# Performance work log

Measured on AMD Instinct MI355X. Metric: run time of the kernel, lower is better.

The kernel has to match this reference:

```python
import jax, jax.numpy as jnp
import numpy as np

D = 768
ED = 192  # d // 4
E = 8     # n_experts
K = 2     # top_k
B, H, W = 32, 32, 32
LN_EPS = 1e-5


def setup_inputs() -> dict:
    key = jax.random.key(0)
    ks = jax.random.split(key, 5)
    s = 0.02
    x = jax.random.normal(ks[0], (B, D, H, W), dtype=jnp.float32)
    Wr = jax.random.normal(ks[1], (E, D), dtype=jnp.float32) * s   # router: logits = tokens @ Wr.T
    W1 = jax.random.normal(ks[2], (E, D, ED), dtype=jnp.float32) * s  # gate proj (silu branch)
    W3 = jax.random.normal(ks[3], (E, D, ED), dtype=jnp.float32) * s  # linear branch
    W2 = jax.random.normal(ks[4], (E, ED, D), dtype=jnp.float32) * s  # down proj
    gamma = jnp.ones((D,), dtype=jnp.float32)
    beta = jnp.zeros((D,), dtype=jnp.float32)
    return {"x": x, "Wr": Wr, "W1": W1, "W3": W3, "W2": W2, "gamma": gamma, "beta": beta}


def _layernorm(y, gamma, beta):
    mu = jnp.mean(y, axis=-1, keepdims=True)
    var = jnp.mean(jnp.square(y - mu), axis=-1, keepdims=True)
    return (y - mu) * jax.lax.rsqrt(var + LN_EPS) * gamma + beta


def _moe_forward(x, Wr, W1, W3, W2, gamma, beta):
    b, c, h, w = x.shape
    tokens = x.transpose(0, 2, 3, 1).reshape(-1, c)        # [T, d]
    logits = tokens @ Wr.T                                  # [T, E]
    topk_v, topk_i = jax.lax.top_k(logits, K)               # [T, K]
    topk_w = jax.nn.softmax(topk_v, axis=-1)                # [T, K]
    # dense combine weights: zero for non-selected experts (same math as masked scatter)
    gates = jnp.sum(jax.nn.one_hot(topk_i, E, dtype=tokens.dtype) * topk_w[..., None], axis=1)  # [T, E]
    # SwiGLU per expert (forward uses silu(e[0](t)) * e[2](t), then e[3])
    hdn = jax.nn.silu(jnp.einsum('td,edh->teh', tokens, W1)) * jnp.einsum('td,edh->teh', tokens, W3)  # [T,E,ed]
    y = jnp.einsum('te,teh,ehd->td', gates, hdn, W2)        # combine: [T, d]
    out = _layernorm(y, gamma, beta) + tokens
    return out.reshape(b, h, w, c).transpose(0, 3, 1, 2)


def reference(x, Wr, W1, W3, W2, gamma, beta):
    return _moe_forward(x, Wr, W1, W3, W2, gamma, beta)
```

## Files before the change

### kernel.cpp

```cpp
#include <hip/hip_runtime.h>
#include <cstdint>
#include <cstddef>

#define T_TOK 32768
#define DM 768
#define EDIM 192
#define NEXP 8

typedef unsigned short u16;
typedef short bf16x8 __attribute__((ext_vector_type(8)));
typedef float f32x4 __attribute__((ext_vector_type(4)));
typedef u16 u16x8 __attribute__((ext_vector_type(8)));

__device__ __forceinline__ u16 f2bf(float f) {
  unsigned u = __float_as_uint(f);
  return (u16)((u + 0x7FFFu + ((u >> 16) & 1u)) >> 16);
}
__device__ __forceinline__ float bf2f(u16 u) {
  return __uint_as_float(((unsigned)u) << 16);
}

__device__ __forceinline__ void gld16(const void* g, void* l) {
  __builtin_amdgcn_global_load_lds(
      (const __attribute__((address_space(1))) unsigned int*)g,
      (__attribute__((address_space(3))) unsigned int*)l,
      16, 0, 0);
}

__device__ __forceinline__ bf16x8 frag_ld(const u16* lds, int row, int kb) {
  int ph = row * 128 + (kb ^ ((row & 7) << 4));
  return *(const bf16x8*)((const char*)lds + ph);
}

__global__ __launch_bounds__(256) void k_prep(
    const float* __restrict__ W1, const float* __restrict__ W3,
    const float* __restrict__ W2, u16* __restrict__ W1T,
    u16* __restrict__ W3T, u16* __restrict__ W2T)
{
  __shared__ __align__(16) float td[64][68];
  const int z = blockIdx.z;
  const int mat = z >> 3, e = z & 7;
  const int R = (mat == 2) ? EDIM : DM;
  const int C = (mat == 2) ? DM : EDIM;
  const int r0 = blockIdx.x * 64, c0 = blockIdx.y * 64;
  if (r0 >= R || c0 >= C) return;
  const float* in = (mat == 0 ? W1 : mat == 1 ? W3 : W2) + (size_t)e * R * C;
  u16* out = (mat == 0 ? W1T : mat == 1 ? W3T : W2T) + (size_t)e * R * C;
  const int tid = threadIdx.x;
  {
    int rl = tid >> 2, cs = (tid & 3) * 16;
    const float* s = in + (size_t)(r0 + rl) * C + c0 + cs;
    #pragma unroll
    for (int i = 0; i < 16; i += 4) *(float4*)&td[rl][cs + i] = *(const float4*)(s + i);
  }
  __syncthreads();
  {
    int cl = tid >> 2, rs = (tid & 3) * 16;
    u16* d = out + (size_t)(c0 + cl) * R + r0 + rs;
    u16x8 o0, o1;
    #pragma unroll
    for (int i = 0; i < 8; ++i) {
      o0[i] = f2bf(td[rs + i][cl]);
      o1[i] = f2bf(td[rs + 8 + i][cl]);
    }
    *(u16x8*)d = o0;
    *(u16x8*)(d + 8) = o1;
  }
}

__global__ __launch_bounds__(256) void k_tokrouter(
    const float* __restrict__ x, const float* __restrict__ Wr,
    u16* __restrict__ tokbf, int* __restrict__ cnt,
    int* __restrict__ toklist, float* __restrict__ gatelist)
{
  __shared__ float WrL[8][772];
  __shared__ float xL[64][33];
  __shared__ float logitsL[32][8];
  __shared__ int cnt8[8];
  __shared__ int baseL[8];
  const int tid = threadIdx.x;
  const int t0 = blockIdx.x * 32;
  const int b = t0 >> 10;
  const int h = (t0 >> 5) & 31;
  const float* xb = x + (size_t)b * (DM * 1024) + h * 32;

  for (int i = tid; i < 1536; i += 256) {
    int r = i / 192;
    int c = (i - r * 192) * 4;
    *(float4*)&WrL[r][c] = ((const float4*)Wr)[i];
  }

  const int rt = tid >> 3;
  const int re = tid & 7;
  float lacc = 0.f;

  for (int cb = 0; cb < 12; ++cb) {
    const int c0 = cb * 64;
    __syncthreads();
    #pragma unroll
    for (int it = 0; it < 2; ++it) {
      int idx = it * 256 + tid;
      int r = idx >> 3, cc = (idx & 7) * 4;
      float4 v = *(const float4*)(xb + (size_t)(c0 + r) * 1024 + cc);
      xL[r][cc] = v.x; xL[r][cc + 1] = v.y; xL[r][cc + 2] = v.z; xL[r][cc + 3] = v.w;
    }
    __syncthreads();
    {
      const float* wr = &WrL[re][c0];
      #pragma unroll
      for (int c = 0; c < 64; ++c) lacc = fmaf(xL[c][rt], wr[c], lacc);
    }
    {
      u16x8 o;
      #pragma unroll
      for (int i = 0; i < 8; ++i) o[i] = f2bf(xL[re * 8 + i][rt]);
      *(u16x8*)(tokbf + (size_t)(t0 + rt) * DM + c0 + re * 8) = o;
    }
  }

  logitsL[rt][re] = lacc;
  if (tid < 8) cnt8[tid] = 0;
  __syncthreads();

  int e0 = -1, e1 = -1, lp0 = 0, lp1 = 0;
  float g0 = 0.f, g1 = 0.f;
  if (tid < 32) {
    float v0 = -1e30f, v1 = -1e30f;
    #pragma unroll
    for (int e = 0; e < 8; ++e) { float v = logitsL[tid][e]; if (v > v0) { v0 = v; e0 = e; } }
    #pragma unroll
    for (int e = 0; e < 8; ++e) {
      if (e == e0) continue;
      float v = logitsL[tid][e]; if (v > v1) { v1 = v; e1 = e; }
    }
    float w = expf(v1 - v0);
    g0 = 1.f / (1.f + w);
    g1 = w / (1.f + w);
    lp0 = atomicAdd(&cnt8[e0], 1);
    lp1 = atomicAdd(&cnt8[e1], 1);
  }
  __syncthreads();
  if (tid < 8) baseL[tid] = atomicAdd(&cnt[tid], cnt8[tid]);
  __syncthreads();
  if (tid < 32) {
    int tg = t0 + tid;
    int p0 = baseL[e0] + lp0;
    int p1 = baseL[e1] + lp1;
    toklist[e0 * T_TOK + p0] = tg;
    gatelist[e0 * T_TOK + p0] = g0;
    toklist[e1 * T_TOK + p1] = tg | (1 << 16);
    gatelist[e1 * T_TOK + p1] = g1;
  }
}

__global__ void k_prefix(const int* __restrict__ cnt, int* __restrict__ offs) {
  if (threadIdx.x == 0) {
    int s = 0;
    for (int e = 0; e < NEXP; ++e) { offs[e] = s; s += cnt[e]; }
    offs[NEXP] = s;
  }
}

__global__ __launch_bounds__(256) void k_ffn1(
    const u16* __restrict__ tokbf, const u16* __restrict__ W1T,
    const u16* __restrict__ W3T, const int* __restrict__ cnt,
    const int* __restrict__ offs, const int* __restrict__ toklist,
    u16* __restrict__ hbuf)
{
  __shared__ __align__(16) u16 As[128 * 64];
  __shared__ __align__(16) u16 B1s[64 * 64];
  __shared__ __align__(16) u16 B3s[64 * 64];
  __shared__ int rowbaseL[128];
  const int e = blockIdx.z;
  const int count = cnt[e];
  const int start = blockIdx.x * 128;
  if (start >= count) return;
  const int n0 = blockIdx.y * 64;
  const int rows = min(128, count - start);
  const int tid = threadIdx.x;

  if (tid < 128) {
    int r = (tid < rows) ? tid : 0;
    rowbaseL[tid] = (toklist[e * T_TOK + start + r] & 0xFFFF) * DM;
  }
  __syncthreads();

  const int lrow = tid >> 3;
  const int swq = (((tid & 7) * 16) ^ ((lrow & 7) << 4)) >> 1;
  const u16 *srcA[4], *srcB1[2], *srcB3[2];
  #pragma unroll
  for (int it = 0; it < 4; ++it)
    srcA[it] = tokbf + rowbaseL[it * 32 + lrow] + swq;
  #pragma unroll
  for (int it = 0; it < 2; ++it) {
    size_t wb = (size_t)(e * EDIM + n0 + it * 32 + lrow) * DM + swq;
    srcB1[it] = W1T + wb;
    srcB3[it] = W3T + wb;
  }

  const int w = tid >> 6, l = tid & 63;
  const int wm = (w >> 1) * 64, wn = (w & 1) * 32;
  const int lr = l & 15;
  const int lk = (l >> 4) * 16;

  f32x4 acc1[4][2], acc3[4][2];
  #pragma unroll
  for (int i = 0; i < 4; ++i)
    #pragma unroll
    for (int j = 0; j < 2; ++j) {
      acc1[i][j] = (f32x4){0.f, 0.f, 0.f, 0.f};
      acc3[i][j] = (f32x4){0.f, 0.f, 0.f, 0.f};
    }

  for (int kc = 0; kc < 12; ++kc) {
    const int ko = kc * 64;
    #pragma unroll
    for (int it = 0; it < 4; ++it)
      gld16(srcA[it] + ko, (char*)As + (it * 256 + tid) * 16);
    #pragma unroll
    for (int it = 0; it < 2; ++it) {
      gld16(srcB1[it] + ko, (char*)B1s + (it * 256 + tid) * 16);
      gld16(srcB3[it] + ko, (char*)B3s + (it * 256 + tid) * 16);
    }
    __syncthreads();
    #pragma unroll
    for (int kk = 0; kk < 2; ++kk) {
      const int kb = kk * 64 + lk;
      bf16x8 af[4], b1[2], b3[2];
      #pragma unroll
      for (int mf = 0; mf < 4; ++mf) af[mf] = frag_ld(As, wm + mf * 16 + lr, kb);
      #pragma unroll
      for (int nf = 0; nf < 2; ++nf) {
        b1[nf] = frag_ld(B1s, wn + nf * 16 + lr, kb);
        b3[nf] = frag_ld(B3s, wn + nf * 16 + lr, kb);
      }
      #pragma unroll
      for (int mf = 0; mf < 4; ++mf)
        #pragma unroll
        for (int nf = 0; nf < 2; ++nf) {
          acc1[mf][nf] = __builtin_amdgcn_mfma_f32_16x16x32_bf16(af[mf], b1[nf], acc1[mf][nf], 0, 0, 0);
          acc3[mf][nf] = __builtin_amdgcn_mfma_f32_16x16x32_bf16(af[mf], b3[nf], acc3[mf][nf], 0, 0, 0);
        }
    }
    __syncthreads();
  }

  const int rq = (l >> 4) * 4;
  const int abase = offs[e] + start;
  #pragma unroll
  for (int mf = 0; mf < 4; ++mf)
    #pragma unroll
    for (int nf = 0; nf < 2; ++nf)
      #pragma unroll
      for (int r = 0; r < 4; ++r) {
        int m = wm + mf * 16 + rq + r;
        if (m < rows) {
          float a = acc1[mf][nf][r];
          float hv = (a / (1.f + expf(-a))) * acc3[mf][nf][r];
          hbuf[(size_t)(abase + m) * EDIM + (n0 + wn + nf * 16 + lr)] = f2bf(hv);
        }
      }
}

__global__ __launch_bounds__(256) void k_ffn2(
    const u16* __restrict__ hbuf, const u16* __restrict__ W2T,
    const int* __restrict__ cnt, const int* __restrict__ offs,
    const int* __restrict__ toklist, const float* __restrict__ gatelist,
    u16* __restrict__ ypart)
{
  __shared__ __align__(16) u16 As[128 * 64];
  __shared__ __align__(16) u16 Bs[128 * 64];
  __shared__ int dstL[128];
  __shared__ float gL[128];
  const int e = blockIdx.z;
  const int count = cnt[e];
  const int start = blockIdx.x * 128;
  if (start >= count) return;
  const int n0 = blockIdx.y * 128;
  const int rows = min(128, count - start);
  const int tid = threadIdx.x;
  const int abase = offs[e] + start;

  if (tid < 128) {
    int r = (tid < rows) ? tid : 0;
    int entry = toklist[e * T_TOK + start + r];
    int t = entry & 0xFFFF, k = entry >> 16;
    dstL[tid] = (k * T_TOK + t) * DM;
    gL[tid] = gatelist[e * T_TOK + start + r];
  }
  __syncthreads();

  const int lrow = tid >> 3;
  const int swq = (((tid & 7) * 16) ^ ((lrow & 7) << 4)) >> 1;
  const u16 *srcA[4], *srcB[4];
  #pragma unroll
  for (int it = 0; it < 4; ++it) {
    int r = it * 32 + lrow;
    int rr = (r < rows) ? r : 0;
    srcA[it] = hbuf + (size_t)(abase + rr) * EDIM + swq;
    srcB[it] = W2T + (size_t)(e * DM + n0 + r) * EDIM + swq;
  }

  const int w = tid >> 6, l = tid & 63;
  const int wm = (w >> 1) * 64, wn = (w & 1) * 64;
  const int lr = l & 15;
  const int lk = (l >> 4) * 16;

  f32x4 acc[4][4];
  #pragma unroll
  for (int i = 0; i < 4; ++i)
    #pragma unroll
    for (int j = 0; j < 4; ++j) acc[i][j] = (f32x4){0.f, 0.f, 0.f, 0.f};

  for (int kc = 0; kc < 3; ++kc) {
    const int ko = kc * 64;
    #pragma unroll
    for (int it = 0; it < 4; ++it) {
      gld16(srcA[it] + ko, (char*)As + (it * 256 + tid) * 16);
      gld16(srcB[it] + ko, (char*)Bs + (it * 256 + tid) * 16);
    }
    __syncthreads();
    #pragma unroll
    for (int kk = 0; kk < 2; ++kk) {
      const int kb = kk * 64 + lk;
      bf16x8 af[4], bf_[4];
      #pragma unroll
      for (int mf = 0; mf < 4; ++mf) af[mf] = frag_ld(As, wm + mf * 16 + lr, kb);
      #pragma unroll
      for (int nf = 0; nf < 4; ++nf) bf_[nf] = frag_ld(Bs, wn + nf * 16 + lr, kb);
      #pragma unroll
      for (int mf = 0; mf < 4; ++mf)
        #pragma unroll
        for (int nf = 0; nf < 4; ++nf)
          acc[mf][nf] = __builtin_amdgcn_mfma_f32_16x16x32_bf16(af[mf], bf_[nf], acc[mf][nf], 0, 0, 0);
    }
    __syncthreads();
  }

  const int rq = (l >> 4) * 4;
  #pragma unroll
  for (int mf = 0; mf < 4; ++mf)
    #pragma unroll
    for (int nf = 0; nf < 4; ++nf)
      #pragma unroll
      for (int r = 0; r < 4; ++r) {
        int m = wm + mf * 16 + rq + r;
        if (m < rows) {
          float v = acc[mf][nf][r] * gL[m];
          ypart[(size_t)dstL[m] + (n0 + wn + nf * 16 + lr)] = f2bf(v);
        }
      }
}

__global__ __launch_bounds__(256) void k_stats(
    const u16* __restrict__ ypart, float* __restrict__ mu, float* __restrict__ rs)
{
  const int tid = threadIdx.x;
  const int t = blockIdx.x * 16 + (tid >> 4);
  const int j = tid & 15;
  const u16* y0 = ypart + (size_t)t * DM;
  const u16* y1 = y0 + (size_t)T_TOK * DM;
  float sum = 0.f, sq = 0.f;
  #pragma unroll
  for (int i = 0; i < 6; ++i) {
    int c = i * 128 + j * 8;
    u16x8 a = *(const u16x8*)(y0 + c);
    u16x8 b = *(const u16x8*)(y1 + c);
    #pragma unroll
    for (int q = 0; q < 8; ++q) {
      float v = bf2f(a[q]) + bf2f(b[q]);
      sum += v; sq += v * v;
    }
  }
  #pragma unroll
  for (int d = 1; d < 16; d <<= 1) { sum += __shfl_xor(sum, d); sq += __shfl_xor(sq, d); }
  if (j == 0) {
    float m = sum * (1.f / 768.f);
    float var = sq * (1.f / 768.f) - m * m;
    mu[t] = m;
    rs[t] = 1.f / sqrtf(var + 1e-5f);
  }
}

__global__ __launch_bounds__(256) void k_apply(
    const u16* __restrict__ ypart, const float* __restrict__ x,
    const float* __restrict__ gamma, const float* __restrict__ beta,
    const float* __restrict__ mu, const float* __restrict__ rs,
    float* __restrict__ out)
{
  __shared__ float lnT[64][65];
  const int tid = threadIdx.x;
  const int t0 = blockIdx.x * 64;
  const int c0 = blockIdx.y * 64;
  const int b = t0 >> 10;
  const int h0 = (t0 >> 5) & 31;
  const u16* y0 = ypart;
  const u16* y1 = ypart + (size_t)T_TOK * DM;
  {
    const int tl = tid >> 2, q = tid & 3;
    const size_t tbase = (size_t)(t0 + tl) * DM;
    const int c = c0 + q * 16;
    const float mu_ = mu[t0 + tl], rs_ = rs[t0 + tl];
    u16x8 a0 = *(const u16x8*)(y0 + tbase + c);
    u16x8 a1 = *(const u16x8*)(y0 + tbase + c + 8);
    u16x8 b0 = *(const u16x8*)(y1 + tbase + c);
    u16x8 b1 = *(const u16x8*)(y1 + tbase + c + 8);
    #pragma unroll
    for (int i = 0; i < 8; ++i) {
      float v = bf2f(a0[i]) + bf2f(b0[i]);
      lnT[q * 16 + i][tl] = (v - mu_) * rs_ * gamma[c + i] + beta[c + i];
      float u = bf2f(a1[i]) + bf2f(b1[i]);
      lnT[q * 16 + 8 + i][tl] = (u - mu_) * rs_ * gamma[c + 8 + i] + beta[c + 8 + i];
    }
  }
  __syncthreads();
  {
    int cl = tid >> 2, ts = (tid & 3) * 16;
    int c = c0 + cl;
    int hh = h0 + (ts >> 5), ww = ts & 31;
    size_t oidx = (((size_t)b * DM + c) * 32 + hh) * 32 + ww;
    #pragma unroll
    for (int i = 0; i < 16; i += 4) {
      float4 xv = *(const float4*)(x + oidx + i);
      float4 ov;
      ov.x = lnT[cl][ts + i + 0] + xv.x;
      ov.y = lnT[cl][ts + i + 1] + xv.y;
      ov.z = lnT[cl][ts + i + 2] + xv.z;
      ov.w = lnT[cl][ts + i + 3] + xv.w;
      *(float4*)(out + oidx + i) = ov;
    }
  }
}

constexpr size_t OFF_TOK  = 0;
constexpr size_t OFF_W1T  = OFF_TOK + (size_t)T_TOK * DM * 2;
constexpr size_t OFF_W3T  = OFF_W1T + (size_t)NEXP * EDIM * DM * 2;
constexpr size_t OFF_W2T  = OFF_W3T + (size_t)NEXP * EDIM * DM * 2;
constexpr size_t OFF_H    = OFF_W2T + (size_t)NEXP * EDIM * DM * 2;
constexpr size_t OFF_YP   = OFF_H + (size_t)T_TOK * 2 * EDIM * 2;
constexpr size_t OFF_CNT  = OFF_YP + (size_t)2 * T_TOK * DM * 2;
constexpr size_t OFF_OFFS = OFF_CNT + 256;
constexpr size_t OFF_LIST = OFF_OFFS + 256;
constexpr size_t OFF_GATE = OFF_LIST + (size_t)NEXP * T_TOK * 4;
constexpr size_t OFF_MU   = OFF_GATE + (size_t)NEXP * T_TOK * 4;
constexpr size_t OFF_RS   = OFF_MU + (size_t)T_TOK * 4;

extern "C" void kernel_launch(void* const* d_in, const int* in_sizes, int n_in,
                              void* d_out, int out_size, void* d_ws, size_t ws_size,
                              hipStream_t stream) {
  const float* x     = (const float*)d_in[0];
  const float* Wr    = (const float*)d_in[1];
  const float* W1    = (const float*)d_in[2];
  const float* W3    = (const float*)d_in[3];
  const float* W2    = (const float*)d_in[4];
  const float* gamma = (const float*)d_in[5];
  const float* beta  = (const float*)d_in[6];
  float* out = (float*)d_out;
  char* ws = (char*)d_ws;

  u16* tokbf = (u16*)(ws + OFF_TOK);
  u16* W1T   = (u16*)(ws + OFF_W1T);
  u16* W3T   = (u16*)(ws + OFF_W3T);
  u16* W2T   = (u16*)(ws + OFF_W2T);
  u16* hbuf  = (u16*)(ws + OFF_H);
  u16* ypart = (u16*)(ws + OFF_YP);
  int* cnt   = (int*)(ws + OFF_CNT);
  int* offs  = (int*)(ws + OFF_OFFS);
  int* toklist = (int*)(ws + OFF_LIST);
  float* gatelist = (float*)(ws + OFF_GATE);
  float* muB = (float*)(ws + OFF_MU);
  float* rsB = (float*)(ws + OFF_RS);

  hipMemsetAsync(cnt, 0, 64, stream);
  hipLaunchKernelGGL(k_prep, dim3(12, 12, 24), dim3(256), 0, stream,
                     W1, W3, W2, W1T, W3T, W2T);
  hipLaunchKernelGGL(k_tokrouter, dim3(1024), dim3(256), 0, stream,
                     x, Wr, tokbf, cnt, toklist, gatelist);
  hipLaunchKernelGGL(k_prefix, dim3(1), dim3(64), 0, stream, cnt, offs);
  hipLaunchKernelGGL(k_ffn1, dim3(256, 3, 8), dim3(256), 0, stream,
                     tokbf, W1T, W3T, cnt, offs, toklist, hbuf);
  hipLaunchKernelGGL(k_ffn2, dim3(256, 6, 8), dim3(256), 0, stream,
                     hbuf, W2T, cnt, offs, toklist, gatelist, ypart);
  hipLaunchKernelGGL(k_stats, dim3(2048), dim3(256), 0, stream,
                     ypart, muB, rsB);
  hipLaunchKernelGGL(k_apply, dim3(512, 12), dim3(256), 0, stream,
                     ypart, x, gamma, beta, muB, rsB, out);
}
```

Measured before the change: 238.3 us.

## Fuse LayerNorm stats and apply, reorder FFN grids, precompute LDS fragment pointers

Merges k_stats and k_apply into one kernel. It stages 32 tokens' summed expert outputs in LDS, computes mean and rstd there, and writes the transposed NCHW output, so ypart is read once instead of twice. The FFN grids now put the expert index on blockIdx.x and the row tile on z, which schedules early tiles of every expert together. LDS fragment addresses are precomputed as fixed pointers instead of recomputing the swizzle per load. The risks are that the sum is rounded to bf16 before normalisation, and that the 50KB LDS tile in the LN kernel lowers occupancy.

```diff
diff --git a/kernel.cpp b/kernel.cpp
--- a/kernel.cpp
+++ b/kernel.cpp
@@ -25,11 +25,6 @@
       (const __attribute__((address_space(1))) unsigned int*)g,
       (__attribute__((address_space(3))) unsigned int*)l,
       16, 0, 0);
-}
-
-__device__ __forceinline__ bf16x8 frag_ld(const u16* lds, int row, int kb) {
-  int ph = row * 128 + (kb ^ ((row & 7) << 4));
-  return *(const bf16x8*)((const char*)lds + ph);
 }
 
 __global__ __launch_bounds__(256) void k_prep(
@@ -171,9 +166,9 @@
   __shared__ __align__(16) u16 B1s[64 * 64];
   __shared__ __align__(16) u16 B3s[64 * 64];
   __shared__ int rowbaseL[128];
-  const int e = blockIdx.z;
+  const int e = blockIdx.x;
   const int count = cnt[e];
-  const int start = blockIdx.x * 128;
+  const int start = blockIdx.z * 128;
   if (start >= count) return;
   const int n0 = blockIdx.y * 64;
   const int rows = min(128, count - start);
@@ -197,11 +192,21 @@
     srcB1[it] = W1T + wb;
     srcB3[it] = W3T + wb;
   }
+  const int dOff = tid * 16;
 
   const int w = tid >> 6, l = tid & 63;
   const int wm = (w >> 1) * 64, wn = (w & 1) * 32;
   const int lr = l & 15;
   const int lk = (l >> 4) * 16;
+  const int sL = (l & 7) << 4;
+  const int o0 = lk ^ sL;
+
+  const char* pA[2]  = { (const char*)As  + (wm + lr) * 128 + o0,
+                         (const char*)As  + (wm + lr) * 128 + (o0 ^ 64) };
+  const char* pB1[2] = { (const char*)B1s + (wn + lr) * 128 + o0,
+                         (const char*)B1s + (wn + lr) * 128 + (o0 ^ 64) };
+  const char* pB3[2] = { (const char*)B3s + (wn + lr) * 128 + o0,
+                         (const char*)B3s + (wn + lr) * 128 + (o0 ^ 64) };
 
   f32x4 acc1[4][2], acc3[4][2];
   #pragma unroll
@@ -216,23 +221,22 @@
     const int ko = kc * 64;
     #pragma unroll
     for (int it = 0; it < 4; ++it)
-      gld16(srcA[it] + ko, (char*)As + (it * 256 + tid) * 16);
+      gld16(srcA[it] + ko, (char*)As + it * 4096 + dOff);
     #pragma unroll
     for (int it = 0; it < 2; ++it) {
-      gld16(srcB1[it] + ko, (char*)B1s + (it * 256 + tid) * 16);
-      gld16(srcB3[it] + ko, (char*)B3s + (it * 256 + tid) * 16);
+      gld16(srcB1[it] + ko, (char*)B1s + it * 4096 + dOff);
+      gld16(srcB3[it] + ko, (char*)B3s + it * 4096 + dOff);
     }
     __syncthreads();
     #pragma unroll
     for (int kk = 0; kk < 2; ++kk) {
-      const int kb = kk * 64 + lk;
       bf16x8 af[4], b1[2], b3[2];
       #pragma unroll
-      for (int mf = 0; mf < 4; ++mf) af[mf] = frag_ld(As, wm + mf * 16 + lr, kb);
+      for (int mf = 0; mf < 4; ++mf) af[mf] = *(const bf16x8*)(pA[kk] + mf * 2048);
       #pragma unroll
       for (int nf = 0; nf < 2; ++nf) {
-        b1[nf] = frag_ld(B1s, wn + nf * 16 + lr, kb);
-        b3[nf] = frag_ld(B3s, wn + nf * 16 + lr, kb);
+        b1[nf] = *(const bf16x8*)(pB1[kk] + nf * 2048);
+        b3[nf] = *(const bf16x8*)(pB3[kk] + nf * 2048);
       }
       #pragma unroll
       for (int mf = 0; mf < 4; ++mf)
@@ -272,9 +276,9 @@
   __shared__ __align__(16) u16 Bs[128 * 64];
   __shared__ int dstL[128];
   __shared__ float gL[128];
-  const int e = blockIdx.z;
+  const int e = blockIdx.x;
   const int count = cnt[e];
-  const int start = blockIdx.x * 128;
+  const int start = blockIdx.z * 128;
   if (start >= count) return;
   const int n0 = blockIdx.y * 128;
   const int rows = min(128, count - start);
@@ -300,11 +304,19 @@
     srcA[it] = hbuf + (size_t)(abase + rr) * EDIM + swq;
     srcB[it] = W2T + (size_t)(e * DM + n0 + r) * EDIM + swq;
   }
+  const int dOff = tid * 16;
 
   const int w = tid >> 6, l = tid & 63;
   const int wm = (w >> 1) * 64, wn = (w & 1) * 64;
   const int lr = l & 15;
   const int lk = (l >> 4) * 16;
+  const int sL = (l & 7) << 4;
+  const int o0 = lk ^ sL;
+
+  const char* pA[2] = { (const char*)As + (wm + lr) * 128 + o0,
+                        (const char*)As + (wm + lr) * 128 + (o0 ^ 64) };
+  const char* pB[2] = { (const char*)Bs + (wn + lr) * 128 + o0,
+                        (const char*)Bs + (wn + lr) * 128 + (o0 ^ 64) };
 
   f32x4 acc[4][4];
   #pragma unroll
@@ -316,18 +328,17 @@
     const int ko = kc * 64;
     #pragma unroll
     for (int it = 0; it < 4; ++it) {
-      gld16(srcA[it] + ko, (char*)As + (it * 256 + tid) * 16);
-      gld16(srcB[it] + ko, (char*)Bs + (it * 256 + tid) * 16);
+      gld16(srcA[it] + ko, (char*)As + it * 4096 + dOff);
+      gld16(srcB[it] + ko, (char*)Bs + it * 4096 + dOff);
     }
     __syncthreads();
     #pragma unroll
     for (int kk = 0; kk < 2; ++kk) {
-      const int kb = kk * 64 + lk;
       bf16x8 af[4], bf_[4];
       #pragma unroll
-      for (int mf = 0; mf < 4; ++mf) af[mf] = frag_ld(As, wm + mf * 16 + lr, kb);
-      #pragma unroll
-      for (int nf = 0; nf < 4; ++nf) bf_[nf] = frag_ld(Bs, wn + nf * 16 + lr, kb);
+      for (int mf = 0; mf < 4; ++mf) af[mf] = *(const bf16x8*)(pA[kk] + mf * 2048);
+      #pragma unroll
+      for (int nf = 0; nf < 4; ++nf) bf_[nf] = *(const bf16x8*)(pB[kk] + nf * 2048);
       #pragma unroll
       for (int mf = 0; mf < 4; ++mf)
         #pragma unroll
@@ -352,82 +363,71 @@
       }
 }
 
-__global__ __launch_bounds__(256) void k_stats(
-    const u16* __restrict__ ypart, float* __restrict__ mu, float* __restrict__ rs)
-{
-  const int tid = threadIdx.x;
-  const int t = blockIdx.x * 16 + (tid >> 4);
-  const int j = tid & 15;
-  const u16* y0 = ypart + (size_t)t * DM;
-  const u16* y1 = y0 + (size_t)T_TOK * DM;
-  float sum = 0.f, sq = 0.f;
-  #pragma unroll
-  for (int i = 0; i < 6; ++i) {
-    int c = i * 128 + j * 8;
-    u16x8 a = *(const u16x8*)(y0 + c);
-    u16x8 b = *(const u16x8*)(y1 + c);
-    #pragma unroll
-    for (int q = 0; q < 8; ++q) {
-      float v = bf2f(a[q]) + bf2f(b[q]);
-      sum += v; sq += v * v;
-    }
-  }
-  #pragma unroll
-  for (int d = 1; d < 16; d <<= 1) { sum += __shfl_xor(sum, d); sq += __shfl_xor(sq, d); }
-  if (j == 0) {
-    float m = sum * (1.f / 768.f);
-    float var = sq * (1.f / 768.f) - m * m;
-    mu[t] = m;
-    rs[t] = 1.f / sqrtf(var + 1e-5f);
-  }
-}
-
-__global__ __launch_bounds__(256) void k_apply(
+__global__ __launch_bounds__(256) void k_lnfused(
     const u16* __restrict__ ypart, const float* __restrict__ x,
     const float* __restrict__ gamma, const float* __restrict__ beta,
-    const float* __restrict__ mu, const float* __restrict__ rs,
     float* __restrict__ out)
 {
-  __shared__ float lnT[64][65];
+  __shared__ u16 yL[32][792];
+  __shared__ float muL[32], rsL[32];
   const int tid = threadIdx.x;
-  const int t0 = blockIdx.x * 64;
-  const int c0 = blockIdx.y * 64;
+  const int t0 = blockIdx.x * 32;
   const int b = t0 >> 10;
-  const int h0 = (t0 >> 5) & 31;
-  const u16* y0 = ypart;
-  const u16* y1 = ypart + (size_t)T_TOK * DM;
+  const int h = (t0 >> 5) & 31;
+  const u16* y0 = ypart + (size_t)t0 * DM;
+  const u16* y1 = y0 + (size_t)T_TOK * DM;
+
+  #pragma unroll
+  for (int i = 0; i < 12; ++i) {
+    int idx = i * 2048 + tid * 8;
+    int t = idx / 768;
+    int c = idx - t * 768;
+    u16x8 a = *(const u16x8*)(y0 + idx);
+    u16x8 d = *(const u16x8*)(y1 + idx);
+    u16x8 o;
+    #pragma unroll
+    for (int q = 0; q < 8; ++q) o[q] = f2bf(bf2f(a[q]) + bf2f(d[q]));
+    *(u16x8*)&yL[t][c] = o;
+  }
+  __syncthreads();
+
   {
-    const int tl = tid >> 2, q = tid & 3;
-    const size_t tbase = (size_t)(t0 + tl) * DM;
-    const int c = c0 + q * 16;
-    const float mu_ = mu[t0 + tl], rs_ = rs[t0 + tl];
-    u16x8 a0 = *(const u16x8*)(y0 + tbase + c);
-    u16x8 a1 = *(const u16x8*)(y0 + tbase + c + 8);
-    u16x8 b0 = *(const u16x8*)(y1 + tbase + c);
-    u16x8 b1 = *(const u16x8*)(y1 + tbase + c + 8);
-    #pragma unroll
-    for (int i = 0; i < 8; ++i) {
-      float v = bf2f(a0[i]) + bf2f(b0[i]);
-      lnT[q * 16 + i][tl] = (v - mu_) * rs_ * gamma[c + i] + beta[c + i];
-      float u = bf2f(a1[i]) + bf2f(b1[i]);
-      lnT[q * 16 + 8 + i][tl] = (u - mu_) * rs_ * gamma[c + 8 + i] + beta[c + 8 + i];
-    }
-  }
-  __syncthreads();
-  {
-    int cl = tid >> 2, ts = (tid & 3) * 16;
-    int c = c0 + cl;
-    int hh = h0 + (ts >> 5), ww = ts & 31;
-    size_t oidx = (((size_t)b * DM + c) * 32 + hh) * 32 + ww;
-    #pragma unroll
-    for (int i = 0; i < 16; i += 4) {
-      float4 xv = *(const float4*)(x + oidx + i);
+    const int tl = tid >> 3, j = tid & 7;
+    float sum = 0.f, sq = 0.f;
+    #pragma unroll
+    for (int i = 0; i < 12; ++i) {
+      u16x8 a = *(const u16x8*)&yL[tl][j * 96 + i * 8];
+      #pragma unroll
+      for (int q = 0; q < 8; ++q) {
+        float v = bf2f(a[q]);
+        sum += v; sq += v * v;
+      }
+    }
+    #pragma unroll
+    for (int d = 1; d < 8; d <<= 1) { sum += __shfl_xor(sum, d); sq += __shfl_xor(sq, d); }
+    if (j == 0) {
+      float m = sum * (1.f / 768.f);
+      float var = sq * (1.f / 768.f) - m * m;
+      muL[tl] = m;
+      rsL[tl] = 1.f / sqrtf(var + 1e-5f);
+    }
+  }
+  __syncthreads();
+
+  #pragma unroll
+  for (int ci = 0; ci < 3; ++ci) {
+    const int c = ci * 256 + tid;
+    const float gc = gamma[c], bc = beta[c];
+    const size_t obase = (((size_t)b * DM + c) * 32 + h) * 32;
+    #pragma unroll
+    for (int jj = 0; jj < 32; jj += 4) {
+      float4 xv = *(const float4*)(x + obase + jj);
       float4 ov;
-      ov.x = lnT[cl][ts + i + 0] + xv.x;
-      ov.y = lnT[cl][ts + i + 1] + xv.y;
-      ov.z = lnT[cl][ts + i + 2] + xv.z;
-      ov.w = lnT[cl][ts + i + 3] + xv.w;
-      *(float4*)(out + oidx + i) = ov;
+      ov.x = (bf2f(yL[jj + 0][c]) - muL[jj + 0]) * rsL[jj + 0] * gc + bc + xv.x;
+      ov.y = (bf2f(yL[jj + 1][c]) - muL[jj + 1]) * rsL[jj + 1] * gc + bc + xv.y;
+      ov.z = (bf2f(yL[jj + 2][c]) - muL[jj + 2]) * rsL[jj + 2] * gc + bc + xv.z;
+      ov.w = (bf2f(yL[jj + 3][c]) - muL[jj + 3]) * rsL[jj + 3] * gc + bc + xv.w;
+      *(float4*)(out + obase + jj) = ov;
     }
   }
 }
@@ -442,8 +442,6 @@
 constexpr size_t OFF_OFFS = OFF_CNT + 256;
 constexpr size_t OFF_LIST = OFF_OFFS + 256;
 constexpr size_t OFF_GATE = OFF_LIST + (size_t)NEXP * T_TOK * 4;
-constexpr size_t OFF_MU   = OFF_GATE + (size_t)NEXP * T_TOK * 4;
-constexpr size_t OFF_RS   = OFF_MU + (size_t)T_TOK * 4;
 
 extern "C" void kernel_launch(void* const* d_in, const int* in_sizes, int n_in,
                               void* d_out, int out_size, void* d_ws, size_t ws_size,
@@ -468,8 +466,6 @@
   int* offs  = (int*)(ws + OFF_OFFS);
   int* toklist = (int*)(ws + OFF_LIST);
   float* gatelist = (float*)(ws + OFF_GATE);
-  float* muB = (float*)(ws + OFF_MU);
-  float* rsB = (float*)(ws + OFF_RS);
 
   hipMemsetAsync(cnt, 0, 64, stream);
   hipLaunchKernelGGL(k_prep, dim3(12, 12, 24), dim3(256), 0, stream,
@@ -477,12 +473,10 @@
   hipLaunchKernelGGL(k_tokrouter, dim3(1024), dim3(256), 0, stream,
                      x, Wr, tokbf, cnt, toklist, gatelist);
   hipLaunchKernelGGL(k_prefix, dim3(1), dim3(64), 0, stream, cnt, offs);
-  hipLaunchKernelGGL(k_ffn1, dim3(256, 3, 8), dim3(256), 0, stream,
+  hipLaunchKernelGGL(k_ffn1, dim3(8, 3, 256), dim3(256), 0, stream,
                      tokbf, W1T, W3T, cnt, offs, toklist, hbuf);
-  hipLaunchKernelGGL(k_ffn2, dim3(256, 6, 8), dim3(256), 0, stream,
+  hipLaunchKernelGGL(k_ffn2, dim3(8, 6, 256), dim3(256), 0, stream,
                      hbuf, W2T, cnt, offs, toklist, gatelist, ypart);
-  hipLaunchKernelGGL(k_stats, dim3(2048), dim3(256), 0, stream,
-                     ypart, muB, rsB);
-  hipLaunchKernelGGL(k_apply, dim3(512, 12), dim3(256), 0, stream,
-                     ypart, x, gamma, beta, muB, rsB, out);
-}
+  hipLaunchKernelGGL(k_lnfused, dim3(1024), dim3(256), 0, stream,
+                     ypart, x, gamma, beta, out);
+}
```

After: 268.8 us. 12.8% more time.
